# Kernel tuning notes

Hardware: AMD Instinct MI355X
Metric: run time of the kernel (lower is better)

## Reference

```python
import jax, jax.numpy as jnp
import numpy as np

B, S, H, NH = 2, 2048, 1024, 16
HD = H // NH  # 64


def setup_inputs() -> dict:
    key = jax.random.key(0)
    ks = jax.random.split(key, 12)
    sc = 0.02
    return {
        "query": jax.random.normal(ks[0], (B, S, H), dtype=jnp.float32),
        "key": jax.random.normal(ks[1], (B, S, H), dtype=jnp.float32),
        "value": jax.random.normal(ks[2], (B, S, H), dtype=jnp.float32),
        "attention_mask": jnp.zeros((B, S, S), dtype=jnp.float32),
        "Wq": jax.random.normal(ks[3], (H, H), dtype=jnp.float32) * sc,
        "bq": jnp.zeros((H,), dtype=jnp.float32),
        "Wk": jax.random.normal(ks[4], (H, H), dtype=jnp.float32) * sc,
        "bk": jnp.zeros((H,), dtype=jnp.float32),
        "Wv": jax.random.normal(ks[5], (H, H), dtype=jnp.float32) * sc,
        "bv": jnp.zeros((H,), dtype=jnp.float32),
        "Wo": jax.random.normal(ks[6], (H, H), dtype=jnp.float32) * sc,
        "bo": jnp.zeros((H,), dtype=jnp.float32),
    }


def reference(query, key, value, attention_mask, Wq, bq, Wk, bk, Wv, bv, Wo, bo):
    b = query.shape[0]
    # linear projections
    q = query @ Wq + bq
    k = key @ Wk + bk
    v = value @ Wv + bv
    # [b, s, h] -> [b, nh, s, hd]
    def split_heads(x):
        return x.reshape(b, -1, NH, HD).transpose(0, 2, 1, 3)
    q, k, v = split_heads(q), split_heads(k), split_heads(v)
    # scaled dot-product attention with materialized score matrix (faithful)
    scores = jnp.einsum("bhqd,bhkd->bhqk", q, k) / jnp.sqrt(jnp.float32(HD))
    scores = scores + attention_mask[:, None, :, :]
    weights = jax.nn.softmax(scores, axis=-1)  # dropout p=0 (eval)
    out = jnp.einsum("bhqk,bhkd->bhqd", weights, v)
    out = out.transpose(0, 2, 1, 3).reshape(b, -1, H)
    return out @ Wo + bo
```

## Files before the change

### kernel.cpp

```cpp
#include <hip/hip_runtime.h>
#include <hip/hip_bf16.h>
#include <math.h>

#define S_  2048
#define H_  1024
#define NH_ 16
#define HD_ 64
#define MM  4096
#define NB_ 2
#define NT_ (S_ / 64)
#define LOG2E 1.44269504088896340736f
#define SMFIX 32.0f

typedef __attribute__((ext_vector_type(8))) short bf16x8;
typedef __attribute__((ext_vector_type(4))) float f32x4;
typedef __attribute__((ext_vector_type(16))) float f32x16;
typedef __attribute__((ext_vector_type(4))) unsigned short us4;
typedef __attribute__((ext_vector_type(8))) unsigned short us8;
typedef __attribute__((ext_vector_type(2))) unsigned uint2v;

__device__ __forceinline__ void gld_lds16(const void* g, void* l) {
    __builtin_amdgcn_global_load_lds(
        (const __attribute__((address_space(1))) unsigned int*)g,
        (__attribute__((address_space(3))) unsigned int*)l, 16, 0, 0);
}

__device__ __forceinline__ unsigned short f2bf(float f) {
    union { float f; unsigned int u; } v; v.f = f;
    unsigned int r = v.u + 0x7FFFu + ((v.u >> 16) & 1u);
    return (unsigned short)(r >> 16);
}

__device__ __forceinline__ unsigned pkbf(float lo, float hi) {
    __hip_bfloat162 h = __float22bfloat162_rn(make_float2(lo, hi));
    unsigned u; __builtin_memcpy(&u, &h, 4); return u;
}

__device__ __forceinline__ float exp2_fast(float x) {
    float r; asm("v_exp_f32 %0, %1" : "=v"(r) : "v"(x)); return r;
}

__global__ __launch_bounds__(256)
void cvt_bf16_3(const float* __restrict__ s0, const float* __restrict__ s1,
                const float* __restrict__ s2, unsigned short* __restrict__ d0,
                unsigned short* __restrict__ d1, unsigned short* __restrict__ d2,
                int n8)
{
    const int z = blockIdx.y;
    const float* s = z == 0 ? s0 : z == 1 ? s1 : s2;
    unsigned short* d = z == 0 ? d0 : z == 1 ? d1 : d2;
    int i = blockIdx.x * 256 + threadIdx.x;
    if (i >= n8) return;
    float4 a = ((const float4*)s)[i * 2];
    float4 b = ((const float4*)s)[i * 2 + 1];
    union { unsigned u[4]; us8 v; } o;
    o.u[0] = pkbf(a.x, a.y); o.u[1] = pkbf(a.z, a.w);
    o.u[2] = pkbf(b.x, b.y); o.u[3] = pkbf(b.z, b.w);
    ((us8*)d)[i] = o.v;
}

__global__ __launch_bounds__(256)
void wtr_kernel(const float* __restrict__ W0, const float* __restrict__ W1,
                const float* __restrict__ W2, const float* __restrict__ W3,
                unsigned short* __restrict__ T0, unsigned short* __restrict__ T1,
                unsigned short* __restrict__ T2, unsigned short* __restrict__ T3)
{
    __shared__ float t[32][33];
    const float* W = blockIdx.z == 0 ? W0 : blockIdx.z == 1 ? W1 : blockIdx.z == 2 ? W2 : W3;
    unsigned short* T = blockIdx.z == 0 ? T0 : blockIdx.z == 1 ? T1 : blockIdx.z == 2 ? T2 : T3;
    const int n0 = blockIdx.x * 32, k0 = blockIdx.y * 32;
    const int tx = threadIdx.x & 31, ty = threadIdx.x >> 5;
    #pragma unroll
    for (int u = 0; u < 4; u++)
        t[ty + u * 8][tx] = W[(size_t)(k0 + ty + u * 8) * H_ + n0 + tx];
    __syncthreads();
    #pragma unroll
    for (int u = 0; u < 4; u++)
        T[(size_t)(n0 + ty + u * 8) * H_ + k0 + tx] = f2bf(t[tx][ty + u * 8]);
}

__global__ __launch_bounds__(256)
void mtr_kernel(const float* __restrict__ M, unsigned short* __restrict__ MT)
{
    __shared__ float t[32][33];
    const int q0 = blockIdx.x * 32, k0 = blockIdx.y * 32, b = blockIdx.z;
    const float* Mb = M + (size_t)b * S_ * S_;
    unsigned short* Tb = MT + (size_t)b * S_ * S_;
    const int tx = threadIdx.x & 31, ty = threadIdx.x >> 5;
    #pragma unroll
    for (int u = 0; u < 4; u++)
        t[ty + u * 8][tx] = Mb[(size_t)(q0 + ty + u * 8) * S_ + k0 + tx];
    __syncthreads();
    #pragma unroll
    for (int u = 0; u < 4; u++)
        Tb[(size_t)(k0 + ty + u * 8) * S_ + q0 + tx] =
            f2bf(fmaf(t[tx][ty + u * 8], LOG2E, -SMFIX));
}

__device__ __forceinline__
void gemm_body(const unsigned short* __restrict__ A, const unsigned short* __restrict__ Bt,
               const float* __restrict__ bias, void* __restrict__ out, float scale, int epi)
{
    __shared__ __align__(16) unsigned short As[128 * 64];
    __shared__ __align__(16) unsigned short Bs[128 * 64];

    const int tid = threadIdx.x;
    const int lane = tid & 63, w = tid >> 6;
    const int lane16 = lane & 15, lg = lane >> 4;
    const int wm = w & 1, wn = w >> 1;
    const int n0 = blockIdx.x * 128, m0 = blockIdx.y * 128;

    f32x4 acc[4][4];
    #pragma unroll
    for (int m = 0; m < 4; m++)
        #pragma unroll
        for (int n = 0; n < 4; n++) acc[m][n] = (f32x4){0.f, 0.f, 0.f, 0.f};

    auto stage = [&](int kt) {
        #pragma unroll
        for (int u = 0; u < 4; u++) {
            const int seg = w * 4 + u;
            const int L = seg * 1024 + lane * 16;
            const int row = L >> 7;
            const int blk = (L >> 4) & 7;
            const int goff = kt * 64 + ((blk ^ (row & 7)) << 3);
            gld_lds16(A  + (size_t)(m0 + row) * 1024 + goff, (char*)As + L);
            gld_lds16(Bt + (size_t)(n0 + row) * 1024 + goff, (char*)Bs + L);
        }
    };

    stage(0);
    for (int kt = 0; kt < 16; kt++) {
        __syncthreads();
        #pragma unroll
        for (int ks = 0; ks < 2; ks++) {
            const int kb = ks * 64 + lg * 16;
            bf16x8 a[4], b[4];
            #pragma unroll
            for (int m = 0; m < 4; m++) {
                const int row = wm * 64 + m * 16 + lane16;
                a[m] = *(const bf16x8*)((const char*)As + row * 128 + (kb ^ ((row & 7) << 4)));
            }
            #pragma unroll
            for (int n = 0; n < 4; n++) {
                const int row = wn * 64 + n * 16 + lane16;
                b[n] = *(const bf16x8*)((const char*)Bs + row * 128 + (kb ^ ((row & 7) << 4)));
            }
            #pragma unroll
            for (int m = 0; m < 4; m++)
                #pragma unroll
                for (int n = 0; n < 4; n++)
                    acc[m][n] = __builtin_amdgcn_mfma_f32_16x16x32_bf16(a[m], b[n], acc[m][n], 0, 0, 0);
        }
        __syncthreads();
        if (kt + 1 < 16) stage(kt + 1);
    }

    #pragma unroll
    for (int n = 0; n < 4; n++) {
        const int col = n0 + wn * 64 + n * 16 + lane16;
        const float bs = bias[col];
        #pragma unroll
        for (int m = 0; m < 4; m++) {
            const int rowb = m0 + wm * 64 + m * 16 + lg * 4;
            if (epi == 0) {
                const int nh = col >> 6, hd = col & 63;
                #pragma unroll
                for (int j = 0; j < 4; j++) {
                    const int row = rowb + j;
                    const int bb = row >> 11, s = row & 2047;
                    ((unsigned short*)out)[((((size_t)bb * NH_ + nh) * S_ + s) << 6) + hd] =
                        f2bf((acc[m][n][j] + bs) * scale);
                }
            } else if (epi == 1) {
                const int nh = col >> 6, hd = col & 63;
                const int bb = rowb >> 11, s = rowb & 2047;
                us4 o;
                #pragma unroll
                for (int j = 0; j < 4; j++) o[j] = f2bf(acc[m][n][j] + bs);
                *(us4*)&((unsigned short*)out)[((((size_t)bb * NH_ + nh) * HD_ + hd) << 11) + s] = o;
            } else {
                #pragma unroll
                for (int j = 0; j < 4; j++)
                    ((float*)out)[(size_t)(rowb + j) * H_ + col] = acc[m][n][j] + bs;
            }
        }
    }
}

__global__ __launch_bounds__(256)
void gemm_qkv(const unsigned short* __restrict__ Xq, const unsigned short* __restrict__ Xk,
              const unsigned short* __restrict__ Xv,
              const unsigned short* __restrict__ Wtq, const unsigned short* __restrict__ Wtk,
              const unsigned short* __restrict__ Wtv,
              const float* __restrict__ bq, const float* __restrict__ bk,
              const float* __restrict__ bv,
              unsigned short* __restrict__ qh, unsigned short* __restrict__ kh,
              unsigned short* __restrict__ vt, float qscale)
{
    const int z = blockIdx.z;
    const unsigned short* A  = z == 0 ? Xq : z == 1 ? Xk : Xv;
    const unsigned short* Bt = z == 0 ? Wtq : z == 1 ? Wtk : Wtv;
    const float* bias        = z == 0 ? bq : z == 1 ? bk : bv;
    void* out                = z == 0 ? (void*)qh : z == 1 ? (void*)kh : (void*)vt;
    gemm_body(A, Bt, bias, out, z == 0 ? qscale : 1.0f, z == 2 ? 1 : 0);
}

__global__ __launch_bounds__(256)
void gemm_out(const unsigned short* __restrict__ A, const unsigned short* __restrict__ Bt,
              const float* __restrict__ bias, float* __restrict__ out)
{
    gemm_body(A, Bt, bias, out, 1.0f, 2);
}

__global__ __launch_bounds__(256, 2)
void mfma_attn(const unsigned short* __restrict__ qh, const unsigned short* __restrict__ kh,
               const unsigned short* __restrict__ vt, const unsigned short* __restrict__ maskT,
               unsigned short* __restrict__ ao)
{
    __shared__ __align__(16) unsigned short Ks[2][64 * 64];
    __shared__ __align__(16) unsigned short Vs[2][64 * 64];

    const int tid = threadIdx.x;
    const int lane = tid & 63, wq = tid >> 6;
    const int l31 = lane & 31, lg2 = lane >> 5;
    const int qt = blockIdx.x, h = blockIdx.y, bz = blockIdx.z;
    const int q = qt * 128 + wq * 32 + l31;

    const unsigned short* Kb = kh + ((size_t)(bz * NH_ + h) * S_) * HD_;
    const unsigned short* Vb = vt + ((size_t)(bz * NH_ + h) * HD_) * S_;
    const unsigned short* MTb = maskT + (size_t)bz * S_ * S_;

    bf16x8 qfrag[4];
    {
        const unsigned short* Qrow = qh + (((size_t)(bz * NH_ + h) * S_) + q) * HD_;
        #pragma unroll
        for (int s = 0; s < 4; s++)
            qfrag[s] = *(const bf16x8*)(Qrow + s * 16 + lg2 * 8);
    }

    auto stageKV = [&](int t) {
        const int buf = t & 1;
        #pragma unroll
        for (int u = 0; u < 2; u++) {
            const int L = u * 4096 + tid * 16;
            const int row = L >> 7, blk = (L >> 4) & 7;
            const int off = (blk ^ (row & 7)) << 3;
            gld_lds16(Kb + (size_t)(t * 64 + row) * HD_ + off, (char*)&Ks[buf][0] + L);
            gld_lds16(Vb + (size_t)row * S_ + t * 64 + off,    (char*)&Vs[buf][0] + L);
        }
    };
    stageKV(0);

    f32x16 mtA[2], mtB[2];
    auto loadMT = [&](int t, f32x16 (&mt)[2]) {
        #pragma unroll
        for (int bb = 0; bb < 2; bb++)
            #pragma unroll
            for (int i = 0; i < 16; i++) {
                const int kvr = t * 64 + bb * 32 + (i & 3) + 8 * (i >> 2) + 4 * lg2;
                const unsigned short mv = MTb[(size_t)kvr * S_ + q];
                mt[bb][i] = __uint_as_float((unsigned)mv << 16);
            }
    };
    loadMT(0, mtA);

    __syncthreads();

    f32x16 oacc[2];
    #pragma unroll
    for (int db = 0; db < 2; db++)
        #pragma unroll
        for (int i = 0; i < 16; i++) oacc[db][i] = 0.f;
    float l_run = 0.f;

    auto tile = [&](int t, f32x16 (&Mc)[2], f32x16 (&Mn)[2]) {
        if (t) __syncthreads();
        const int buf = t & 1;

        if (t + 1 < NT_) { stageKV(t + 1); loadMT(t + 1, Mn); }

        f32x16 sc[2];
        __builtin_amdgcn_s_setprio(1);
        #pragma unroll
        for (int bb = 0; bb < 2; bb++) {
            f32x16 a;
            #pragma unroll
            for (int i = 0; i < 16; i++) a[i] = 0.f;
            #pragma unroll
            for (int s = 0; s < 4; s++) {
                const int row = bb * 32 + l31;
                bf16x8 kf = *(const bf16x8*)((const char*)&Ks[buf][0] + row * 128 +
                                             ((s * 32 + lg2 * 16) ^ ((row & 7) << 4)));
                a = __builtin_amdgcn_mfma_f32_32x32x16_bf16(kf, qfrag[s], a, 0, 0, 0);
            }
            sc[bb] = a;
        }
        __builtin_amdgcn_s_setprio(0);

        #pragma unroll
        for (int bb = 0; bb < 2; bb++)
            #pragma unroll
            for (int i = 0; i < 16; i++)
                sc[bb][i] = exp2_fast(sc[bb][i] + Mc[bb][i]);
        float s8[8];
        #pragma unroll
        for (int i = 0; i < 8; i++)
            s8[i] = (sc[0][i] + sc[0][i + 8]) + (sc[1][i] + sc[1][i + 8]);
        l_run += ((s8[0] + s8[1]) + (s8[2] + s8[3])) + ((s8[4] + s8[5]) + (s8[6] + s8[7]));

        bf16x8 pfrag[4];
        #pragma unroll
        for (int bb = 0; bb < 2; bb++)
            #pragma unroll
            for (int g = 0; g < 2; g++) {
                const int o = g * 8;
                unsigned X0 = pkbf(sc[bb][o + 0], sc[bb][o + 1]);
                unsigned X1 = pkbf(sc[bb][o + 2], sc[bb][o + 3]);
                unsigned Y0 = pkbf(sc[bb][o + 4], sc[bb][o + 5]);
                unsigned Y1 = pkbf(sc[bb][o + 6], sc[bb][o + 7]);
                uint2v r0 = __builtin_amdgcn_permlane32_swap(X0, Y0, false, false);
                uint2v r1 = __builtin_amdgcn_permlane32_swap(X1, Y1, false, false);
                union { unsigned u[4]; bf16x8 v; } P;
                P.u[0] = r0.x; P.u[1] = r1.x; P.u[2] = r0.y; P.u[3] = r1.y;
                pfrag[bb * 2 + g] = P.v;
            }

        __builtin_amdgcn_s_setprio(1);
        #pragma unroll
        for (int s = 0; s < 4; s++)
            #pragma unroll
            for (int db = 0; db < 2; db++) {
                const int row = db * 32 + l31;
                bf16x8 vf = *(const bf16x8*)((const char*)&Vs[buf][0] + row * 128 +
                                             ((s * 32 + lg2 * 16) ^ ((row & 7) << 4)));
                oacc[db] = __builtin_amdgcn_mfma_f32_32x32x16_bf16(vf, pfrag[s], oacc[db], 0, 0, 0);
            }
        __builtin_amdgcn_s_setprio(0);
    };

    for (int tt = 0; tt < NT_; tt += 2) {
        tile(tt,     mtA, mtB);
        tile(tt + 1, mtB, mtA);
    }

    l_run += __shfl_xor(l_run, 32, 64);
    const float inv = 1.0f / l_run;
    unsigned short* aoq = ao + ((size_t)(bz * S_ + q)) * H_ + h * HD_;
    #pragma unroll
    for (int db = 0; db < 2; db++)
        #pragma unroll
        for (int m = 0; m < 4; m++) {
            us4 o = { f2bf(oacc[db][m * 4 + 0] * inv), f2bf(oacc[db][m * 4 + 1] * inv),
                      f2bf(oacc[db][m * 4 + 2] * inv), f2bf(oacc[db][m * 4 + 3] * inv) };
            *(us4*)&aoq[db * 32 + m * 8 + lg2 * 4] = o;
        }
}

extern "C" void kernel_launch(void* const* d_in, const int* in_sizes, int n_in,
                              void* d_out, int out_size, void* d_ws, size_t ws_size,
                              hipStream_t stream)
{
    (void)in_sizes; (void)n_in; (void)out_size; (void)ws_size;

    const float* query = (const float*)d_in[0];
    const float* key   = (const float*)d_in[1];
    const float* value = (const float*)d_in[2];
    const float* mask  = (const float*)d_in[3];
    const float* Wq    = (const float*)d_in[4];
    const float* bq    = (const float*)d_in[5];
    const float* Wk    = (const float*)d_in[6];
    const float* bk    = (const float*)d_in[7];
    const float* Wv    = (const float*)d_in[8];
    const float* bv    = (const float*)d_in[9];
    const float* Wo    = (const float*)d_in[10];
    const float* bo    = (const float*)d_in[11];

    unsigned short* ws = (unsigned short*)d_ws;
    const size_t MH = (size_t)MM * H_;
    const size_t WW = (size_t)H_ * H_;
    unsigned short* Xq  = ws;
    unsigned short* Xk  = Xq + MH;
    unsigned short* Xv  = Xk + MH;
    unsigned short* Wtq = Xv + MH;
    unsigned short* Wtk = Wtq + WW;
    unsigned short* Wtv = Wtk + WW;
    unsigned short* Wto = Wtv + WW;
    unsigned short* qh  = Wto + WW;
    unsigned short* kh  = qh + MH;
    unsigned short* vt  = kh + MH;
    unsigned short* ao  = vt + MH;
    unsigned short* maskT = Xq;

    const int n8 = (int)(MH / 8);
    cvt_bf16_3<<<dim3(n8 / 256, 3), 256, 0, stream>>>(query, key, value, Xq, Xk, Xv, n8);
    wtr_kernel<<<dim3(32, 32, 4), 256, 0, stream>>>(Wq, Wk, Wv, Wo, Wtq, Wtk, Wtv, Wto);

    gemm_qkv<<<dim3(8, 32, 3), 256, 0, stream>>>(Xq, Xk, Xv, Wtq, Wtk, Wtv,
                                                 bq, bk, bv, qh, kh, vt, 0.125f * LOG2E);

    mtr_kernel<<<dim3(S_ / 32, S_ / 32, NB_), 256, 0, stream>>>(mask, maskT);

    mfma_attn<<<dim3(S_ / 128, NH_, NB_), 256, 0, stream>>>(qh, kh, vt, maskT, ao);

    gemm_out<<<dim3(8, 32), 256, 0, stream>>>(ao, Wto, bo, (float*)d_out);
}
```

Baseline: 162.8 us.

## Pre-swizzle mask into MFMA fragment order for vectorized attention loads

The mask preprocessing kernel now writes the bf16 log2-scaled mask in a layout that matches each lane's MFMA accumulator element order, 16 contiguous values per lane per 32-row block. The attention kernel then loads its mask fragments with four 16-byte vector loads per tile instead of 32 scattered 2-byte loads, and keeps them packed in registers, unpacking bf16 to float with shifts and masks. This cuts memory instruction count and register pressure in the attention loop. In exchange the transpose kernel has a more complex indexing scheme, and the register unpacking adds a few ALU ops.

Result: faster. 148.7 us (-8.7%).

```diff
diff --git a/kernel.cpp b/kernel.cpp
--- a/kernel.cpp
+++ b/kernel.cpp
@@ -80,21 +80,37 @@
 }
 
 __global__ __launch_bounds__(256)
-void mtr_kernel(const float* __restrict__ M, unsigned short* __restrict__ MT)
-{
-    __shared__ float t[32][33];
-    const int q0 = blockIdx.x * 32, k0 = blockIdx.y * 32, b = blockIdx.z;
+void mtr_kernel(const float* __restrict__ M, unsigned short* __restrict__ MT2)
+{
+    __shared__ float t[64][33];
+    const int q0 = blockIdx.x * 64, t2 = blockIdx.y, b = blockIdx.z;
+    const int kv0 = (t2 >> 1) * 64 + (t2 & 1) * 32;
     const float* Mb = M + (size_t)b * S_ * S_;
-    unsigned short* Tb = MT + (size_t)b * S_ * S_;
-    const int tx = threadIdx.x & 31, ty = threadIdx.x >> 5;
-    #pragma unroll
-    for (int u = 0; u < 4; u++)
-        t[ty + u * 8][tx] = Mb[(size_t)(q0 + ty + u * 8) * S_ + k0 + tx];
+    const int tid = threadIdx.x;
+
+    #pragma unroll
+    for (int u = 0; u < 2; u++) {
+        const int f4 = tid + u * 256;
+        const int r = f4 >> 3, c = (f4 & 7) * 4;
+        float4 v = *(const float4*)(Mb + (size_t)(q0 + r) * S_ + kv0 + c);
+        t[r][c + 0] = v.x; t[r][c + 1] = v.y; t[r][c + 2] = v.z; t[r][c + 3] = v.w;
+    }
     __syncthreads();
-    #pragma unroll
-    for (int u = 0; u < 4; u++)
-        Tb[(size_t)(k0 + ty + u * 8) * S_ + q0 + tx] =
-            f2bf(fmaf(t[tx][ty + u * 8], LOG2E, -SMFIX));
+
+    const int lg2 = tid >> 7, rem = tid & 127;
+    const int q = rem >> 1, half = rem & 1;
+    union { unsigned u[4]; us8 v; } o;
+    #pragma unroll
+    for (int w = 0; w < 4; w++) {
+        const int i0 = half * 8 + 2 * w;
+        const int kc0 = (i0 & 3) + 8 * (i0 >> 2) + 4 * lg2;
+        const int i1 = i0 + 1;
+        const int kc1 = (i1 & 3) + 8 * (i1 >> 2) + 4 * lg2;
+        o.u[w] = pkbf(fmaf(t[q][kc0], LOG2E, -SMFIX),
+                      fmaf(t[q][kc1], LOG2E, -SMFIX));
+    }
+    const size_t flat = ((((size_t)b * 64 + t2) * 2 + lg2) * 2048 + (q0 + q)) * 16 + half * 8;
+    *(us8*)(MT2 + flat) = o.v;
 }
 
 __device__ __forceinline__
@@ -229,7 +245,7 @@
 
     const unsigned short* Kb = kh + ((size_t)(bz * NH_ + h) * S_) * HD_;
     const unsigned short* Vb = vt + ((size_t)(bz * NH_ + h) * HD_) * S_;
-    const unsigned short* MTb = maskT + (size_t)bz * S_ * S_;
+    const unsigned short* MT2b = maskT + (size_t)bz * S_ * S_;
 
     bf16x8 qfrag[4];
     {
@@ -252,18 +268,17 @@
     };
     stageKV(0);
 
-    f32x16 mtA[2], mtB[2];
-    auto loadMT = [&](int t, f32x16 (&mt)[2]) {
-        #pragma unroll
-        for (int bb = 0; bb < 2; bb++)
-            #pragma unroll
-            for (int i = 0; i < 16; i++) {
-                const int kvr = t * 64 + bb * 32 + (i & 3) + 8 * (i >> 2) + 4 * lg2;
-                const unsigned short mv = MTb[(size_t)kvr * S_ + q];
-                mt[bb][i] = __uint_as_float((unsigned)mv << 16);
-            }
+    us8 mpA[2][2], mpB[2][2];
+    auto loadMT = [&](int t, us8 (&mp)[2][2]) {
+        #pragma unroll
+        for (int bb = 0; bb < 2; bb++) {
+            const unsigned short* src = MT2b +
+                ((((size_t)(t * 2 + bb)) * 2 + lg2) * 2048 + q) * 16;
+            mp[bb][0] = *(const us8*)(src);
+            mp[bb][1] = *(const us8*)(src + 8);
+        }
     };
-    loadMT(0, mtA);
+    loadMT(0, mpA);
 
     __syncthreads();
 
@@ -274,7 +289,7 @@
         for (int i = 0; i < 16; i++) oacc[db][i] = 0.f;
     float l_run = 0.f;
 
-    auto tile = [&](int t, f32x16 (&Mc)[2], f32x16 (&Mn)[2]) {
+    auto tile = [&](int t, us8 (&Mc)[2][2], us8 (&Mn)[2][2]) {
         if (t) __syncthreads();
         const int buf = t & 1;
 
@@ -299,10 +314,17 @@
         __builtin_amdgcn_s_setprio(0);
 
         #pragma unroll
-        for (int bb = 0; bb < 2; bb++)
-            #pragma unroll
-            for (int i = 0; i < 16; i++)
-                sc[bb][i] = exp2_fast(sc[bb][i] + Mc[bb][i]);
+        for (int bb = 0; bb < 2; bb++) {
+            union { us8 v; unsigned u[4]; } h0, h1;
+            h0.v = Mc[bb][0]; h1.v = Mc[bb][1];
+            #pragma unroll
+            for (int i = 0; i < 16; i++) {
+                const unsigned wrd = (i < 8) ? h0.u[i >> 1] : h1.u[(i - 8) >> 1];
+                const float mf = __uint_as_float((i & 1) ? (wrd & 0xFFFF0000u)
+                                                         : (wrd << 16));
+                sc[bb][i] = exp2_fast(sc[bb][i] + mf);
+            }
+        }
         float s8[8];
         #pragma unroll
         for (int i = 0; i < 8; i++)
@@ -340,8 +362,8 @@
     };
 
     for (int tt = 0; tt < NT_; tt += 2) {
-        tile(tt,     mtA, mtB);
-        tile(tt + 1, mtB, mtA);
+        tile(tt,     mpA, mpB);
+        tile(tt + 1, mpB, mpA);
     }
 
     l_run += __shfl_xor(l_run, 32, 64);
@@ -399,7 +421,7 @@
     gemm_qkv<<<dim3(8, 32, 3), 256, 0, stream>>>(Xq, Xk, Xv, Wtq, Wtk, Wtv,
                                                  bq, bk, bv, qh, kh, vt, 0.125f * LOG2E);
 
-    mtr_kernel<<<dim3(S_ / 32, S_ / 32, NB_), 256, 0, stream>>>(mask, maskT);
+    mtr_kernel<<<dim3(S_ / 64, 64, NB_), 256, 0, stream>>>(mask, maskT);
 
     mfma_attn<<<dim3(S_ / 128, NH_, NB_), 256, 0, stream>>>(qh, kh, vt, maskT, ao);
 
```
